# Kernel tuning notes

Measured on AMD Instinct MI355X. Metric: run time of the kernel, lower is better.

Reference implementation:

```python
import jax, jax.numpy as jnp
import numpy as np

RRELU_SLOPE = (1.0 / 8.0 + 1.0 / 3.0) / 2.0  # F.rrelu eval mode
N_ENT, N_REL2, H, E, B, T = 20000, 460, 128, 400000, 1024, 8


def _lin(x, W, b):
    return x @ W.T + b  # torch nn.Linear convention


def _gru_cell(x, h, w_ih, w_hh, b_ih, b_hh):
    gi = x @ w_ih.T + b_ih
    gh = h @ w_hh.T + b_hh
    i_r, i_z, i_n = jnp.split(gi, 3, axis=1)
    h_r, h_z, h_n = jnp.split(gh, 3, axis=1)
    r = jax.nn.sigmoid(i_r + h_r)
    z = jax.nn.sigmoid(i_z + h_z)
    n = jnp.tanh(i_n + r * h_n)
    return (1.0 - z) * n + z * h


def setup_inputs() -> dict:
    key = jax.random.key(0)
    ks = jax.random.split(key, 24)
    s = 0.02
    inp = {
        'ent_emb': jax.random.normal(ks[0], (N_ENT, H), jnp.float32),
        'rel_emb': jax.random.normal(ks[1], (N_REL2, H), jnp.float32),
        'weight_neighbor': jax.random.normal(ks[2], (H, H), jnp.float32) * s,
        'loop_weight': jax.random.normal(ks[3], (H, H), jnp.float32) * s,
        'evolve_loop_weight': jax.random.normal(ks[4], (H, H), jnp.float32) * s,
        'w_ih': jax.random.normal(ks[5], (3 * H, H), jnp.float32) * s,
        'w_hh': jax.random.normal(ks[6], (3 * H, H), jnp.float32) * s,
        'b_ih': jnp.zeros((3 * H,), jnp.float32),
        'b_hh': jnp.zeros((3 * H,), jnp.float32),
        'W_map1': jax.random.normal(ks[7], (2 * H, H), jnp.float32) * s,
        'b_map1': jnp.zeros((2 * H,), jnp.float32),
        'W_map2': jax.random.normal(ks[8], (H, 2 * H), jnp.float32) * s,
        'b_map2': jnp.zeros((H,), jnp.float32),
        'W_h1': jax.random.normal(ks[9], (H, H), jnp.float32) * s,
        'b_h1': jnp.zeros((H,), jnp.float32),
        'W_h2': jax.random.normal(ks[10], (H, H), jnp.float32) * s,
        'b_h2': jnp.zeros((H,), jnp.float32),
        'W_align': jax.random.normal(ks[11], (H, H), jnp.float32) * s,
        'b_align': jnp.zeros((H,), jnp.float32),
        'W_attn': jax.random.normal(ks[12], (H, H), jnp.float32) * s,
        'b_attn': jnp.zeros((H,), jnp.float32),
    }
    u = jax.random.uniform(ks[13], (B, T * N_REL2), jnp.float32)
    mask = jax.random.uniform(ks[14], (B, T * N_REL2)) > 0.7  # sparse history
    inp['partial_embeding'] = u * mask
    inp['edge_src'] = jax.random.randint(ks[15], (E,), 0, N_ENT, jnp.int32)
    inp['edge_dst'] = jax.random.randint(ks[16], (E,), 0, N_ENT, jnp.int32)
    inp['edge_type'] = jax.random.randint(ks[17], (E,), 0, N_REL2, jnp.int32)
    sub = jax.random.randint(ks[18], (B,), 0, N_ENT, jnp.int32)
    rel = jax.random.randint(ks[19], (B,), 0, N_REL2, jnp.int32)
    obj = jax.random.randint(ks[20], (B,), 0, N_ENT, jnp.int32)
    inp['triples'] = jnp.stack([sub, rel, obj], axis=1)
    return inp


def reference(ent_emb, rel_emb, weight_neighbor, loop_weight, evolve_loop_weight,
              w_ih, w_hh, b_ih, b_hh, W_map1, b_map1, W_map2, b_map2,
              W_h1, b_h1, W_h2, b_h2, W_align, b_align, W_attn, b_attn,
              partial_embeding, edge_src, edge_dst, edge_type, triples):
    # ---- UnionRGCNLayer: gather-transform-scatter ----
    h = ent_emb
    msg = (h[edge_src] + rel_emb[edge_type]) @ weight_neighbor          # [E, H]
    agg = jax.ops.segment_sum(msg, edge_dst, num_segments=N_ENT)        # [N, H]
    deg = jax.ops.segment_sum(jnp.ones((edge_dst.shape[0],), h.dtype), edge_dst,
                              num_segments=N_ENT)
    norm = jnp.where(deg > 0, 1.0 / jnp.where(deg > 0, deg, 1.0), 0.0)[:, None]
    loop = jnp.where((deg > 0)[:, None], h @ loop_weight, h @ evolve_loop_weight)
    x = agg * norm + loop
    pre_emb = jnp.where(x >= 0, x, x * RRELU_SLOPE)                     # rrelu (eval)

    # ---- PathPredictor.forward_back ----
    mapped_rel = _lin(_lin(rel_emb, W_map1, b_map1), W_map2, b_map2)    # [2R, H]
    q_rel = mapped_rel[triples[:, 1]]                                   # [B, H]
    A = _lin(q_rel, W_attn, b_attn) @ mapped_rel.T                      # [B, 2R]
    hist = partial_embeding.reshape(B, T, N_REL2).transpose(1, 0, 2)    # [T, B, 2R]

    def step(gh, cur):
        attn = cur * A
        attn = jax.nn.softmax(jnp.where(attn == 0, -1e9, attn), axis=1)
        rel_path = attn @ mapped_rel                                    # [B, H]
        return _gru_cell(rel_path, gh, w_ih, w_hh, b_ih, b_hh), None

    gru_hidden, _ = jax.lax.scan(step, jnp.zeros((B, H), pre_emb.dtype), hist)
    predicted_hist = 0.1 * _lin(_lin(q_rel, W_h1, b_h1), W_h2, b_h2) + q_rel
    match_loss = jnp.mean((predicted_hist - gru_hidden) ** 2)

    # ---- forward_forth, distmult scoring ----
    gh2 = _gru_cell(q_rel, predicted_hist, w_ih, w_hh, b_ih, b_hh)      # [B, H]
    sub_emb = pre_emb[triples[:, 0]]
    aligned_all = _lin(pre_emb, W_align, b_align)                       # [N, H]
    score_ = (_lin(sub_emb, W_align, b_align) * gh2) @ aligned_all.T    # [B, N]
    score = jax.nn.sigmoid(score_)
    # BCE(score, one_hot(obj)) without materializing labels:
    logp = jax.nn.log_sigmoid(score_)
    log1mp = jax.nn.log_sigmoid(-score_)
    total = -jnp.sum(log1mp)
    rows = jnp.arange(B)
    total = total + jnp.sum(log1mp[rows, triples[:, 2]] - logp[rows, triples[:, 2]])
    path_loss = total / (B * N_ENT)
    return score, match_loss, path_loss
```

## Files before the change

kernel.cpp:

```cpp
#include <hip/hip_runtime.h>

typedef unsigned short u16;
typedef unsigned int u32;
typedef __attribute__((ext_vector_type(8))) short bf8v;
typedef __attribute__((ext_vector_type(4))) float f4v;

#define RRELU_SLOPE 0.22916666667f

__device__ inline float bf2f(u16 u){ unsigned int i = ((unsigned int)u) << 16; float f; __builtin_memcpy(&f, &i, 4); return f; }
__device__ inline u16 f2bf(float f){ unsigned int i; __builtin_memcpy(&i, &f, 4); unsigned int r = (i + 0x7fffu + ((i >> 16) & 1u)) >> 16; return (u16)r; }
__device__ inline float frcp(float x){ return __builtin_amdgcn_rcpf(x); }
__device__ inline float fsigm(float x){ return frcp(1.f + __expf(-x)); }
__device__ inline float ftanh(float x){ return 2.f * frcp(1.f + __expf(-2.f * x)) - 1.f; }

__global__ __launch_bounds__(256) void prep_k(
    const float* __restrict__ Wn, const float* __restrict__ Wl, const float* __restrict__ We,
    const float* __restrict__ wih, const float* __restrict__ whh,
    const float* __restrict__ m1, const float* __restrict__ m2,
    const float* __restrict__ h1, const float* __restrict__ h2,
    const float* __restrict__ attn, const float* __restrict__ alg, const float* __restrict__ rel,
    const float* __restrict__ ent, const float* __restrict__ bat, const float* __restrict__ bh1,
    const int* __restrict__ edst, int E,
    u16* __restrict__ Bcat, u16* __restrict__ wihb, u16* __restrict__ whhb,
    u16* __restrict__ m1b, u16* __restrict__ m2b, u16* __restrict__ h1b, u16* __restrict__ h2b,
    u16* __restrict__ attnb, u16* __restrict__ algb, u16* __restrict__ relb,
    u16* __restrict__ entb, float* __restrict__ bias2, int* __restrict__ hist)
{
    int id = blockIdx.x * 256 + threadIdx.x;
    if (id < 49152) {
        int n = id / 384, k = id % 384;
        float v = (k < 128) ? Wn[k*128 + n] : (k < 256 ? Wl[(k-128)*128 + n] : We[(k-256)*128 + n]);
        Bcat[id] = f2bf(v); return;
    }
    id -= 49152;
    if (id < 49152) { wihb[id] = f2bf(wih[id]); return; } id -= 49152;
    if (id < 49152) { whhb[id] = f2bf(whh[id]); return; } id -= 49152;
    if (id < 32768) { m1b[id]  = f2bf(m1[id]);  return; } id -= 32768;
    if (id < 32768) { m2b[id]  = f2bf(m2[id]);  return; } id -= 32768;
    if (id < 16384) { h1b[id]  = f2bf(h1[id]);  return; } id -= 16384;
    if (id < 16384) { h2b[id]  = f2bf(h2[id]);  return; } id -= 16384;
    if (id < 16384) { attnb[id]= f2bf(attn[id]);return; } id -= 16384;
    if (id < 16384) { algb[id] = f2bf(alg[id]); return; } id -= 16384;
    if (id < 58880) { relb[id] = f2bf(rel[id]); return; } id -= 58880;
    if (id < 2560000) { entb[id] = f2bf(ent[id]); return; } id -= 2560000;
    if (id < 256) { bias2[id] = (id < 128) ? bat[id] : bh1[id - 128]; return; } id -= 256;
    if (id < E) atomicAdd(&hist[edst[id]], 1);
}

__global__ __launch_bounds__(1024) void scan_k(
    const int* __restrict__ hist, int* __restrict__ starts, int* __restrict__ cursor)
{
    __shared__ int part[1024];
    int t = threadIdx.x;
    int base = t * 20;
    int s = 0;
    for (int j = 0; j < 20; ++j) { int idx = base + j; if (idx < 20000) s += hist[idx]; }
    part[t] = s;
    __syncthreads();
    for (int off = 1; off < 1024; off <<= 1) {
        int v = (t >= off) ? part[t - off] : 0;
        __syncthreads();
        part[t] += v;
        __syncthreads();
    }
    int run = (t > 0) ? part[t - 1] : 0;
    for (int j = 0; j < 20; ++j) {
        int idx = base + j;
        if (idx < 20000) { starts[idx] = run; cursor[idx] = run; run += hist[idx]; }
    }
    if (t == 1023) starts[20000] = run;
}

__global__ __launch_bounds__(256) void scatter_k(
    const int* __restrict__ src, const int* __restrict__ dst, const int* __restrict__ typ,
    int* __restrict__ cursor, int2* __restrict__ spack, int E)
{
    int e = blockIdx.x * 256 + threadIdx.x;
    if (e >= E) return;
    int d = dst[e];
    int p = atomicAdd(&cursor[d], 1);
    spack[p] = make_int2(src[e], typ[e]);
}

__global__ __launch_bounds__(64) void agg_acat_k(
    const int2* __restrict__ spack, const int* __restrict__ starts,
    const u32* __restrict__ hb, const u32* __restrict__ rb, u32* __restrict__ Acat32)
{
    int i = blockIdx.x;
    int lane = threadIdx.x;
    int s0 = starts[i], s1 = starts[i + 1];
    float sx = 0.f, sy = 0.f;
    int e = s0;
    for (; e + 4 <= s1; e += 4) {
        int2 st0 = spack[e], st1 = spack[e+1], st2 = spack[e+2], st3 = spack[e+3];
        u32 a0 = hb[(long)st0.x * 64 + lane]; u32 r0 = rb[(long)st0.y * 64 + lane];
        u32 a1 = hb[(long)st1.x * 64 + lane]; u32 r1 = rb[(long)st1.y * 64 + lane];
        u32 a2 = hb[(long)st2.x * 64 + lane]; u32 r2 = rb[(long)st2.y * 64 + lane];
        u32 a3 = hb[(long)st3.x * 64 + lane]; u32 r3 = rb[(long)st3.y * 64 + lane];
        sx += bf2f((u16)(a0 & 0xffff)) + bf2f((u16)(r0 & 0xffff));
        sy += bf2f((u16)(a0 >> 16))    + bf2f((u16)(r0 >> 16));
        sx += bf2f((u16)(a1 & 0xffff)) + bf2f((u16)(r1 & 0xffff));
        sy += bf2f((u16)(a1 >> 16))    + bf2f((u16)(r1 >> 16));
        sx += bf2f((u16)(a2 & 0xffff)) + bf2f((u16)(r2 & 0xffff));
        sy += bf2f((u16)(a2 >> 16))    + bf2f((u16)(r2 >> 16));
        sx += bf2f((u16)(a3 & 0xffff)) + bf2f((u16)(r3 & 0xffff));
        sy += bf2f((u16)(a3 >> 16))    + bf2f((u16)(r3 >> 16));
    }
    for (; e < s1; ++e) {
        int2 st = spack[e];
        u32 a = hb[(long)st.x * 64 + lane];
        u32 r = rb[(long)st.y * 64 + lane];
        sx += bf2f((u16)(a & 0xffff)) + bf2f((u16)(r & 0xffff));
        sy += bf2f((u16)(a >> 16))    + bf2f((u16)(r >> 16));
    }
    bool has = s1 > s0;
    float nrm = has ? frcp((float)(s1 - s0)) : 0.f;
    u32 hv = hb[(long)i * 64 + lane];
    u32 agg = (u32)f2bf(sx * nrm) | ((u32)f2bf(sy * nrm) << 16);
    long o = (long)i * 192 + lane;
    Acat32[o]       = agg;
    Acat32[o + 64]  = has ? hv : 0u;
    Acat32[o + 128] = has ? 0u : hv;
}

__global__ __launch_bounds__(256) void gemm_nt(
    const u16* __restrict__ A, const u16* __restrict__ B, const float* __restrict__ bias,
    float* __restrict__ Cf, u16* __restrict__ Cbf, u16* __restrict__ CT,
    const u16* __restrict__ residb, const int* __restrict__ arows,
    int M, int N, int K, int lda, int ldb, int ldc, int ldct, int arow_stride,
    float rscale, int epi)
{
    int tid = threadIdx.x;
    int wave = tid >> 6, lane = tid & 63;
    int ln = lane & 15, q = lane >> 4;
    int bm = blockIdx.y * 64 + wave * 16;
    int bn = blockIdx.x * 64;
    int am = bm + ln; if (am >= M) am = M - 1;
    long ar = arows ? (long)arows[(long)am * arow_stride] : (long)am;
    const u16* Ap = A + ar * lda;
    int br[4];
#pragma unroll
    for (int nt = 0; nt < 4; ++nt) { int n = bn + nt*16 + ln; br[nt] = (n < N) ? n : (N - 1); }
    f4v acc[4] = {};
    for (int kc = 0; kc < K; kc += 32) {
        bf8v af = *(const bf8v*)(Ap + kc + q*8);
#pragma unroll
        for (int nt = 0; nt < 4; ++nt) {
            bf8v bv = *(const bf8v*)(B + (long)br[nt]*ldb + kc + q*8);
            acc[nt] = __builtin_amdgcn_mfma_f32_16x16x32_bf16(af, bv, acc[nt], 0, 0, 0);
        }
    }
#pragma unroll
    for (int nt = 0; nt < 4; ++nt) {
        int n = bn + nt*16 + ln;
        if (n >= N) continue;
        float bv = bias ? bias[n] : 0.f;
#pragma unroll
        for (int r = 0; r < 4; ++r) {
            int m = bm + q*4 + r;
            if (m >= M) continue;
            float v = acc[nt][r] + bv;
            if (epi == 1) v = (v >= 0.f) ? v : v * RRELU_SLOPE;
            if (residb)  v = rscale * v + bf2f(residb[(long)m*ldc + n]);
            long ci = (long)m*ldc + n;
            if (Cf)  Cf[ci]  = v;
            if (Cbf) Cbf[ci] = f2bf(v);
            if (CT)  CT[(long)n*ldct + m] = f2bf(v);
        }
    }
}

__global__ __launch_bounds__(256) void fuse_map_k(
    const u16* __restrict__ relb, const u16* __restrict__ m1b, const float* __restrict__ bm1,
    const u16* __restrict__ m2b, const float* __restrict__ bm2,
    u16* __restrict__ mapb, u16* __restrict__ mapT)
{
    __shared__ u16 t1l[4][16][264];
    int tid = threadIdx.x;
    int wave = tid >> 6, lane = tid & 63;
    int ln = lane & 15, q = lane >> 4;
    int base = blockIdx.x * 64 + wave * 16;
    int arow = base + ln; if (arow > 459) arow = 459;
    const u16* Ap = relb + arow * 128;
    f4v acc1[16] = {};
    for (int kc = 0; kc < 128; kc += 32) {
        bf8v af = *(const bf8v*)(Ap + kc + q*8);
#pragma unroll
        for (int nt = 0; nt < 16; ++nt) {
            bf8v bv = *(const bf8v*)(m1b + (nt*16 + ln)*128 + kc + q*8);
            acc1[nt] = __builtin_amdgcn_mfma_f32_16x16x32_bf16(af, bv, acc1[nt], 0, 0, 0);
        }
    }
#pragma unroll
    for (int nt = 0; nt < 16; ++nt) {
        int n = nt*16 + ln;
        float bv = bm1[n];
#pragma unroll
        for (int r = 0; r < 4; ++r)
            t1l[wave][q*4 + r][n] = f2bf(acc1[nt][r] + bv);
    }
    f4v acc2[8] = {};
    for (int kc = 0; kc < 256; kc += 32) {
        bf8v af = *(const bf8v*)&t1l[wave][ln][kc + q*8];
#pragma unroll
        for (int nt = 0; nt < 8; ++nt) {
            bf8v bv = *(const bf8v*)(m2b + (nt*16 + ln)*256 + kc + q*8);
            acc2[nt] = __builtin_amdgcn_mfma_f32_16x16x32_bf16(af, bv, acc2[nt], 0, 0, 0);
        }
    }
#pragma unroll
    for (int nt = 0; nt < 8; ++nt) {
        int n = nt*16 + ln;
        float bv = bm2[n];
#pragma unroll
        for (int r = 0; r < 4; ++r) {
            int m = base + q*4 + r;
            if (m < 460) {
                u16 hv = f2bf(acc2[nt][r] + bv);
                mapb[m*128 + n] = hv;
                mapT[n*480 + m] = hv;
            }
        }
    }
}

__global__ __launch_bounds__(256) void fuse_qt_k(
    const u16* __restrict__ mapb, const int* __restrict__ trip,
    const u16* __restrict__ atb, const float* __restrict__ bias2,
    const u16* __restrict__ h2b, const float* __restrict__ bh2,
    u16* __restrict__ atq, float* __restrict__ pred, u16* __restrict__ X)
{
    __shared__ u16 th1l[4][16][136];
    int tid = threadIdx.x;
    int wave = tid >> 6, lane = tid & 63;
    int ln = lane & 15, q = lane >> 4;
    int base = blockIdx.x * 64 + wave * 16;
    int ar = trip[(base + ln)*3 + 1];
    const u16* Ap = mapb + ar * 128;
    int rm_[4];
#pragma unroll
    for (int r = 0; r < 4; ++r) rm_[r] = trip[(base + q*4 + r)*3 + 1];
    f4v acc1[16] = {};
    for (int kc = 0; kc < 128; kc += 32) {
        bf8v af = *(const bf8v*)(Ap + kc + q*8);
#pragma unroll
        for (int nt = 0; nt < 16; ++nt) {
            bf8v bv = *(const bf8v*)(atb + (nt*16 + ln)*128 + kc + q*8);
            acc1[nt] = __builtin_amdgcn_mfma_f32_16x16x32_bf16(af, bv, acc1[nt], 0, 0, 0);
        }
    }
#pragma unroll
    for (int nt = 0; nt < 16; ++nt) {
        int n = nt*16 + ln;
        float bv = bias2[n];
#pragma unroll
        for (int r = 0; r < 4; ++r) {
            int m = base + q*4 + r;
            float x = acc1[nt][r] + bv;
            if (nt < 8) {
                atq[m*128 + n] = f2bf(x);
                X[(long)(8192 + m)*128 + n] = mapb[rm_[r]*128 + n];
            } else th1l[wave][q*4 + r][n - 128] = f2bf(x);
        }
    }
    f4v acc2[8] = {};
    for (int kc = 0; kc < 128; kc += 32) {
        bf8v af = *(const bf8v*)&th1l[wave][ln][kc + q*8];
#pragma unroll
        for (int nt = 0; nt < 8; ++nt) {
            bf8v bv = *(const bf8v*)(h2b + (nt*16 + ln)*128 + kc + q*8);
            acc2[nt] = __builtin_amdgcn_mfma_f32_16x16x32_bf16(af, bv, acc2[nt], 0, 0, 0);
        }
    }
#pragma unroll
    for (int nt = 0; nt < 8; ++nt) {
        int n = nt*16 + ln;
        float bv = bh2[n];
#pragma unroll
        for (int r = 0; r < 4; ++r) {
            int m = base + q*4 + r;
            pred[(long)m*128 + n] = 0.1f * (acc2[nt][r] + bv) + bf2f(mapb[rm_[r]*128 + n]);
        }
    }
}

__global__ __launch_bounds__(256) void smrp_k(
    const float* __restrict__ Amat, const float* __restrict__ part,
    const u16* __restrict__ mapT, u16* __restrict__ X)
{
    __shared__ u16 xls[32][488];
    __shared__ float asl[4][464];
    int tid = threadIdx.x;
    int wave = tid >> 6, lane = tid & 63;
    int b0 = blockIdx.x * 4;
    for (int i = tid; i < 4*460; i += 256)
        asl[i/460][i%460] = Amat[(long)(b0 + i/460)*460 + i%460];
    __syncthreads();
    for (int j = 0; j < 8; ++j) {
        int rl = wave*8 + j;
        int t = rl >> 2, db = rl & 3;
        const float* crow = part + (long)(b0 + db)*3680 + t*460;
        float v[8], e[8];
        float m = -1e30f;
#pragma unroll
        for (int i = 0; i < 8; ++i) {
            int r = i*64 + lane;
            if (r < 460) {
                float x = crow[r] * asl[db][r];
                x = (x == 0.f) ? -1e9f : x;
                v[i] = x; m = fmaxf(m, x);
            } else v[i] = -1e30f;
        }
#pragma unroll
        for (int off = 32; off; off >>= 1) m = fmaxf(m, __shfl_xor(m, off));
        float sum = 0.f;
#pragma unroll
        for (int i = 0; i < 8; ++i) {
            int r = i*64 + lane;
            e[i] = 0.f;
            if (r < 460) { e[i] = __expf(v[i] - m); sum += e[i]; }
        }
#pragma unroll
        for (int off = 32; off; off >>= 1) sum += __shfl_xor(sum, off);
        float inv = frcp(sum);
#pragma unroll
        for (int i = 0; i < 8; ++i) {
            int r = i*64 + lane;
            if (r < 460)      xls[rl][r] = f2bf(e[i] * inv);
            else if (r < 488) xls[rl][r] = 0;
        }
    }
    __syncthreads();
    int ln = lane & 15, q = lane >> 4;
    f4v acc[2][2] = {};
    for (int kc = 0; kc < 480; kc += 32) {
        bf8v a[2], bfr[2];
#pragma unroll
        for (int mt = 0; mt < 2; ++mt)
            a[mt] = *(const bf8v*)&xls[mt*16 + ln][kc + q*8];
#pragma unroll
        for (int nt = 0; nt < 2; ++nt)
            bfr[nt] = *(const bf8v*)(mapT + (wave*32 + nt*16 + ln)*480 + kc + q*8);
#pragma unroll
        for (int mt = 0; mt < 2; ++mt)
#pragma unroll
            for (int nt = 0; nt < 2; ++nt)
                acc[mt][nt] = __builtin_amdgcn_mfma_f32_16x16x32_bf16(a[mt], bfr[nt], acc[mt][nt], 0, 0, 0);
    }
#pragma unroll
    for (int mt = 0; mt < 2; ++mt)
#pragma unroll
    for (int nt = 0; nt < 2; ++nt) {
        int n = wave*32 + nt*16 + ln;
#pragma unroll
        for (int r = 0; r < 4; ++r) {
            int rl = mt*16 + q*4 + r;
            long m = (long)(rl >> 2)*1024 + b0 + (rl & 3);
            X[m*128 + n] = f2bf(acc[mt][nt][r]);
        }
    }
}

__global__ __launch_bounds__(256, 1) void gru_k(
    const u16* __restrict__ X, const u16* __restrict__ wihb, const float* __restrict__ bih,
    const u16* __restrict__ whhb, const float* __restrict__ bhh,
    const float* __restrict__ pred, const float* __restrict__ subl,
    const u16* __restrict__ AL, const int* __restrict__ trip,
    u16* __restrict__ V, float* __restrict__ accp)
{
    __shared__ u16  hbf[16][136];
    __shared__ float hf [4][128];
    __shared__ float ghl[4][388];
    __shared__ float gil[4][388];
    __shared__ float redm[4], redo[4];
    int tid = threadIdx.x;
    int wave = tid >> 6, lane = tid & 63;
    int ln = lane & 15, q = lane >> 4;
    int bb = blockIdx.x * 4;
    for (int i = tid; i < 16*136; i += 256) hbf[i/136][i%136] = 0;
    for (int i = tid; i < 4*128; i += 256) hf[i>>7][i&127] = 0.f;
    bf8v bfrag[6][4], wfrag[6][4];
#pragma unroll
    for (int nt = 0; nt < 6; ++nt)
#pragma unroll
        for (int kc = 0; kc < 4; ++kc) {
            bfrag[nt][kc] = *(const bf8v*)(whhb + (long)(wave*96 + nt*16 + ln)*128 + kc*32 + q*8);
            wfrag[nt][kc] = *(const bf8v*)(wihb + (long)(wave*96 + nt*16 + ln)*128 + kc*32 + q*8);
        }
    int k = tid & 127;
    float cr = bih[k] + bhh[k];
    float cz = bih[128 + k] + bhh[128 + k];
    float bin_ = bih[256 + k], bhn = bhh[256 + k];
    __syncthreads();
    float msum = 0.f, osum = 0.f;
    for (int t = 0; t <= 8; ++t) {
        float pv[2];
#pragma unroll
        for (int it = 0; it < 2; ++it) {
            int m = it*2 + (tid >> 7);
            pv[it] = (t >= 7) ? pred[(long)(bb + m)*128 + k] : 0.f;
        }
        if (t == 8) {
#pragma unroll
            for (int it = 0; it < 2; ++it) {
                int m = it*2 + (tid >> 7);
                hf[m][k] = pv[it]; hbf[m][k] = f2bf(pv[it]);
            }
            __syncthreads();
        }
        long xr0 = (t < 8) ? ((long)t*1024 + bb) : (long)(8192 + bb);
        const u16* Xp = X + (xr0 + (ln & 3))*128;
        f4v gacc[6] = {};
        f4v acc[6] = {};
#pragma unroll
        for (int kc = 0; kc < 4; ++kc) {
            bf8v xf = *(const bf8v*)(Xp + kc*32 + q*8);
            bf8v af = *(const bf8v*)&hbf[ln][kc*32 + q*8];
#pragma unroll
            for (int nt = 0; nt < 6; ++nt) {
                gacc[nt] = __builtin_amdgcn_mfma_f32_16x16x32_bf16(xf, wfrag[nt][kc], gacc[nt], 0, 0, 0);
                acc[nt]  = __builtin_amdgcn_mfma_f32_16x16x32_bf16(af, bfrag[nt][kc], acc[nt],  0, 0, 0);
            }
        }
        if (q == 0) {
#pragma unroll
            for (int nt = 0; nt < 6; ++nt)
#pragma unroll
                for (int r = 0; r < 4; ++r) {
                    ghl[r][wave*96 + nt*16 + ln] = acc[nt][r];
                    gil[r][wave*96 + nt*16 + ln] = gacc[nt][r];
                }
        }
        __syncthreads();
#pragma unroll
        for (int it = 0; it < 2; ++it) {
            int m = it*2 + (tid >> 7);
            float rr = fsigm(gil[m][k] + ghl[m][k] + cr);
            float zz = fsigm(gil[m][128 + k] + ghl[m][128 + k] + cz);
            float nn = ftanh(gil[m][256 + k] + bin_ + rr * (ghl[m][256 + k] + bhn));
            float hn = (1.f - zz) * nn + zz * hf[m][k];
            if (t == 7) { float d = pv[it] - hn; msum += d*d; }
            if (t == 8) {
                u16 vb = f2bf(subl[(long)(bb + m)*128 + k] * hn);
                V[(long)(bb + m)*128 + k] = vb;
                int obj = trip[(bb + m)*3 + 2];
                osum += bf2f(vb) * bf2f(AL[(long)obj*128 + k]);
            } else { hf[m][k] = hn; hbf[m][k] = f2bf(hn); }
        }
        __syncthreads();
    }
#pragma unroll
    for (int off = 32; off; off >>= 1) { msum += __shfl_down(msum, off); osum += __shfl_down(osum, off); }
    if (lane == 0) { redm[wave] = msum; redo[wave] = osum; }
    __syncthreads();
    if (tid == 0) {
        atomicAdd(accp + 0, redm[0] + redm[1] + redm[2] + redm[3]);
        atomicAdd(accp + 2, -(redo[0] + redo[1] + redo[2] + redo[3]));
    }
}

__global__ __launch_bounds__(512) void score_k(
    const u16* __restrict__ V, const u16* __restrict__ AL,
    float* __restrict__ out, float* __restrict__ sp_acc, int N)
{
    __shared__ float stage[8][2048];
    int tid = threadIdx.x;
    int wave = tid >> 6, lane = tid & 63;
    int ln = lane & 15, q = lane >> 4;
    int bm = blockIdx.y * 128 + (wave >> 2) * 64;
    int bn = blockIdx.x * 128 + (wave & 3) * 32;
    bool valid = bn < N;
    int br[2];
#pragma unroll
    for (int nt = 0; nt < 2; ++nt) { int n = bn + nt*16 + ln; br[nt] = (n < N) ? n : (N - 1); }
    f4v acc[4][2] = {};
    for (int kc = 0; kc < 128; kc += 32) {
        bf8v a[4], b[2];
#pragma unroll
        for (int mt = 0; mt < 4; ++mt)
            a[mt] = *(const bf8v*)(V + (long)(bm + mt*16 + ln)*128 + kc + q*8);
#pragma unroll
        for (int nt = 0; nt < 2; ++nt)
            b[nt] = *(const bf8v*)(AL + (long)br[nt]*128 + kc + q*8);
#pragma unroll
        for (int mt = 0; mt < 4; ++mt)
#pragma unroll
            for (int nt = 0; nt < 2; ++nt)
                acc[mt][nt] = __builtin_amdgcn_mfma_f32_16x16x32_bf16(a[mt], b[nt], acc[mt][nt], 0, 0, 0);
    }
    float lsum = 0.f;
    float* st = stage[wave];
#pragma unroll
    for (int mt = 0; mt < 4; ++mt)
#pragma unroll
    for (int nt = 0; nt < 2; ++nt)
#pragma unroll
    for (int r = 0; r < 4; ++r) {
        float s = acc[mt][nt][r];
        float e = __expf(-fabsf(s));
        float d = 1.f + e;
        float inv = frcp(d);
        st[(mt*16 + q*4 + r)*32 + nt*16 + ln] = (s >= 0.f) ? inv : e * inv;
        lsum += fmaxf(s, 0.f) + __logf(d);
    }
    if (!valid) lsum = 0.f;
    if (valid) {
        int row0 = lane >> 3, c4 = (lane & 7) << 2;
#pragma unroll
        for (int i = 0; i < 8; ++i) {
            int row = i*8 + row0;
            f4v vv = *(const f4v*)&st[row*32 + c4];
            __builtin_nontemporal_store(vv, (f4v*)&out[(long)(bm + row)*N + bn + c4]);
        }
    }
#pragma unroll
    for (int off = 32; off; off >>= 1) lsum += __shfl_xor(lsum, off);
    __shared__ float red[8];
    if (lane == 0) red[wave] = lsum;
    __syncthreads();
    if (tid == 0) {
        float tsum = 0.f;
#pragma unroll
        for (int w = 0; w < 8; ++w) tsum += red[w];
        atomicAdd(sp_acc, tsum);
    }
}

__global__ void final_k(const float* __restrict__ acc, float* __restrict__ out)
{
    out[20480000] = acc[0] / (1024.f * 128.f);
    out[20480001] = (acc[1] + acc[2]) / (1024.f * 20000.f);
}

extern "C" void kernel_launch(void* const* d_in, const int* in_sizes, int n_in,
                              void* d_out, int out_size, void* d_ws, size_t ws_size,
                              hipStream_t stream)
{
    const float* ent  = (const float*)d_in[0];
    const float* rel  = (const float*)d_in[1];
    const float* Wn   = (const float*)d_in[2];
    const float* Wl   = (const float*)d_in[3];
    const float* We   = (const float*)d_in[4];
    const float* wih  = (const float*)d_in[5];
    const float* whh  = (const float*)d_in[6];
    const float* b_ih = (const float*)d_in[7];
    const float* b_hh = (const float*)d_in[8];
    const float* Wm1  = (const float*)d_in[9];
    const float* bm1  = (const float*)d_in[10];
    const float* Wm2  = (const float*)d_in[11];
    const float* bm2  = (const float*)d_in[12];
    const float* Wh1  = (const float*)d_in[13];
    const float* bh1  = (const float*)d_in[14];
    const float* Wh2  = (const float*)d_in[15];
    const float* bh2  = (const float*)d_in[16];
    const float* Wal  = (const float*)d_in[17];
    const float* bal  = (const float*)d_in[18];
    const float* Wat  = (const float*)d_in[19];
    const float* bat  = (const float*)d_in[20];
    const float* part = (const float*)d_in[21];
    const int* esrc   = (const int*)d_in[22];
    const int* edst   = (const int*)d_in[23];
    const int* etyp   = (const int*)d_in[24];
    const int* trip   = (const int*)d_in[25];
    float* out = (float*)d_out;
    const int E = in_sizes[22];

    char* ws = (char*)d_ws;
    size_t off = 0;
    auto alloc = [&](size_t bytes) { size_t o = off; off = (off + bytes + 255) & ~(size_t)255; return o; };

    size_t o_acc   = alloc(256);
    size_t o_hist  = alloc(20000 * 4);
    size_t o_mapT  = alloc(128 * 480 * 2);
    size_t zend = off;
    size_t o_starts= alloc(20004 * 4);
    size_t o_cur   = alloc(20000 * 4);
    size_t o_spack = alloc((size_t)E * 8);
    size_t o_entb  = alloc((size_t)20000 * 128 * 2);
    size_t o_acat  = alloc((size_t)20000 * 384 * 2);
    size_t o_pre   = alloc((size_t)20000 * 128 * 2);
    size_t o_aln   = alloc((size_t)20000 * 128 * 2);
    size_t o_bcat  = alloc(128 * 384 * 2);
    size_t o_wih   = alloc(384 * 128 * 2);
    size_t o_whh   = alloc(384 * 128 * 2);
    size_t o_m1    = alloc(256 * 128 * 2);
    size_t o_m2    = alloc(128 * 256 * 2);
    size_t o_ath   = alloc(2 * 128 * 128 * 2);
    size_t o_h2    = alloc(128 * 128 * 2);
    size_t o_al    = alloc(128 * 128 * 2);
    size_t o_rel   = alloc(460 * 128 * 2);
    size_t o_map   = alloc(460 * 128 * 2);
    size_t o_atq   = alloc(1024 * 128 * 2);
    size_t o_b2    = alloc(256 * 4);
    size_t o_pred  = alloc(1024 * 128 * 4);
    size_t o_amat  = alloc((size_t)1024 * 460 * 4);
    size_t o_X     = alloc((size_t)9216 * 128 * 2);
    size_t o_subl  = alloc(1024 * 128 * 4);
    size_t o_V     = alloc(1024 * 128 * 2);

    float* accp  = (float*)(ws + o_acc);
    int* histp   = (int*)(ws + o_hist);
    u16* mapT    = (u16*)(ws + o_mapT);
    int* startsp = (int*)(ws + o_starts);
    int* curp    = (int*)(ws + o_cur);
    int2* spack  = (int2*)(ws + o_spack);
    u16* entb    = (u16*)(ws + o_entb);
    u16* acat    = (u16*)(ws + o_acat);
    u16* preb    = (u16*)(ws + o_pre);
    u16* alnb    = (u16*)(ws + o_aln);
    u16* bcat    = (u16*)(ws + o_bcat);
    u16* wihb    = (u16*)(ws + o_wih);
    u16* whhb    = (u16*)(ws + o_whh);
    u16* m1b     = (u16*)(ws + o_m1);
    u16* m2b     = (u16*)(ws + o_m2);
    u16* atb     = (u16*)(ws + o_ath);
    u16* h1b     = atb + 128 * 128;
    u16* h2b     = (u16*)(ws + o_h2);
    u16* alb     = (u16*)(ws + o_al);
    u16* relb    = (u16*)(ws + o_rel);
    u16* mapb    = (u16*)(ws + o_map);
    u16* atqb    = (u16*)(ws + o_atq);
    float* bias2 = (float*)(ws + o_b2);
    float* predf = (float*)(ws + o_pred);
    float* amat  = (float*)(ws + o_amat);
    u16* Xb      = (u16*)(ws + o_X);
    float* subl  = (float*)(ws + o_subl);
    u16* Vb      = (u16*)(ws + o_V);

    hipMemsetAsync(ws, 0, zend, stream);

    int ptot = 2897664 + E;
    prep_k<<<(ptot + 255) / 256, 256, 0, stream>>>(
        Wn, Wl, We, wih, whh, Wm1, Wm2, Wh1, Wh2, Wat, Wal, rel,
        ent, bat, bh1, edst, E,
        bcat, wihb, whhb, m1b, m2b, h1b, h2b, atb, alb, relb,
        entb, bias2, histp);

    scan_k<<<1, 1024, 0, stream>>>(histp, startsp, curp);
    int eb = (E + 255) / 256;
    scatter_k<<<eb, 256, 0, stream>>>(esrc, edst, etyp, curp, spack, E);
    agg_acat_k<<<20000, 64, 0, stream>>>(spack, startsp, (const u32*)entb, (const u32*)relb, (u32*)acat);

    gemm_nt<<<dim3(2, 313), 256, 0, stream>>>(acat, bcat, nullptr, nullptr, preb, nullptr, nullptr, nullptr,
                                              20000, 128, 384, 384, 384, 128, 0, 0, 0.f, 1);
    gemm_nt<<<dim3(2, 313), 256, 0, stream>>>(preb, alb, bal, nullptr, alnb, nullptr, nullptr, nullptr,
                                              20000, 128, 128, 128, 128, 128, 0, 0, 0.f, 0);

    fuse_map_k<<<8, 256, 0, stream>>>(relb, m1b, bm1, m2b, bm2, mapb, mapT);

    fuse_qt_k<<<16, 256, 0, stream>>>(mapb, trip, atb, bias2, h2b, bh2, atqb, predf, Xb);

    gemm_nt<<<dim3(8, 16), 256, 0, stream>>>(atqb, mapb, nullptr, amat, nullptr, nullptr, nullptr, nullptr,
                                             1024, 460, 128, 128, 128, 460, 0, 0, 0.f, 0);

    smrp_k<<<256, 256, 0, stream>>>(amat, part, mapT, Xb);

    gemm_nt<<<dim3(2, 16), 256, 0, stream>>>(preb, alb, bal, subl, nullptr, nullptr, nullptr, trip,
                                             1024, 128, 128, 128, 128, 128, 0, 3, 0.f, 0);

    gru_k<<<256, 256, 0, stream>>>(Xb, wihb, b_ih, whhb, b_hh, predf, subl, alnb, trip, Vb, accp);

    score_k<<<dim3(157, 8), 512, 0, stream>>>(Vb, alnb, out, accp + 1, 20000);

    final_k<<<1, 1, 0, stream>>>(accp, out);

    (void)in_sizes; (void)n_in; (void)out_size; (void)ws_size;
}
```

Baseline: 436.9 us.

## Fuse GEMMs into consumer kernels and drop generic gemm_nt launches

Fuses the two back-to-back 20000-row GEMMs (pre-embedding with RReLU, then the align projection) into one kernel that keeps the RReLU tile in shared memory for the second MFMA pass. Also computes the attention-query times mapped-relation GEMM inside smrp_k, and the subject-align linear inside gru_k, which removes the amat and subl intermediate buffers and three kernel launches. The aim is to cut launch overhead and global round-trips. In exchange some work is duplicated or done with lower MFMA utilisation: smrp_k uses only 4 of 16 MFMA rows, and each block reloads weight fragments.

```diff
diff --git a/kernel.cpp b/kernel.cpp
--- a/kernel.cpp
+++ b/kernel.cpp
@@ -123,49 +123,57 @@
     Acat32[o + 128] = has ? 0u : hv;
 }
 
-__global__ __launch_bounds__(256) void gemm_nt(
-    const u16* __restrict__ A, const u16* __restrict__ B, const float* __restrict__ bias,
-    float* __restrict__ Cf, u16* __restrict__ Cbf, u16* __restrict__ CT,
-    const u16* __restrict__ residb, const int* __restrict__ arows,
-    int M, int N, int K, int lda, int ldb, int ldc, int ldct, int arow_stride,
-    float rscale, int epi)
-{
+__global__ __launch_bounds__(256) void prealn_k(
+    const u16* __restrict__ acat, const u16* __restrict__ bcat,
+    const u16* __restrict__ alb, const float* __restrict__ bal,
+    u16* __restrict__ preb, u16* __restrict__ alnb)
+{
+    __shared__ u16 pl[4][16][136];
     int tid = threadIdx.x;
     int wave = tid >> 6, lane = tid & 63;
     int ln = lane & 15, q = lane >> 4;
-    int bm = blockIdx.y * 64 + wave * 16;
-    int bn = blockIdx.x * 64;
-    int am = bm + ln; if (am >= M) am = M - 1;
-    long ar = arows ? (long)arows[(long)am * arow_stride] : (long)am;
-    const u16* Ap = A + ar * lda;
-    int br[4];
-#pragma unroll
-    for (int nt = 0; nt < 4; ++nt) { int n = bn + nt*16 + ln; br[nt] = (n < N) ? n : (N - 1); }
-    f4v acc[4] = {};
-    for (int kc = 0; kc < K; kc += 32) {
+    int bm = blockIdx.x * 64 + wave * 16;
+    int am = bm + ln; if (am > 19999) am = 19999;
+    const u16* Ap = acat + (long)am * 384;
+    f4v acc[8] = {};
+    for (int kc = 0; kc < 384; kc += 32) {
         bf8v af = *(const bf8v*)(Ap + kc + q*8);
 #pragma unroll
-        for (int nt = 0; nt < 4; ++nt) {
-            bf8v bv = *(const bf8v*)(B + (long)br[nt]*ldb + kc + q*8);
+        for (int nt = 0; nt < 8; ++nt) {
+            bf8v bv = *(const bf8v*)(bcat + (nt*16 + ln)*384 + kc + q*8);
             acc[nt] = __builtin_amdgcn_mfma_f32_16x16x32_bf16(af, bv, acc[nt], 0, 0, 0);
         }
     }
 #pragma unroll
-    for (int nt = 0; nt < 4; ++nt) {
-        int n = bn + nt*16 + ln;
-        if (n >= N) continue;
-        float bv = bias ? bias[n] : 0.f;
+    for (int nt = 0; nt < 8; ++nt) {
+        int n = nt*16 + ln;
 #pragma unroll
         for (int r = 0; r < 4; ++r) {
             int m = bm + q*4 + r;
-            if (m >= M) continue;
-            float v = acc[nt][r] + bv;
-            if (epi == 1) v = (v >= 0.f) ? v : v * RRELU_SLOPE;
-            if (residb)  v = rscale * v + bf2f(residb[(long)m*ldc + n]);
-            long ci = (long)m*ldc + n;
-            if (Cf)  Cf[ci]  = v;
-            if (Cbf) Cbf[ci] = f2bf(v);
-            if (CT)  CT[(long)n*ldct + m] = f2bf(v);
+            float v = acc[nt][r];
+            v = (v >= 0.f) ? v : v * RRELU_SLOPE;
+            u16 hv = f2bf(v);
+            pl[wave][q*4 + r][n] = hv;
+            if (m < 20000) preb[(long)m*128 + n] = hv;
+        }
+    }
+    f4v acc2[8] = {};
+    for (int kc = 0; kc < 128; kc += 32) {
+        bf8v af = *(const bf8v*)&pl[wave][ln][kc + q*8];
+#pragma unroll
+        for (int nt = 0; nt < 8; ++nt) {
+            bf8v bv = *(const bf8v*)(alb + (nt*16 + ln)*128 + kc + q*8);
+            acc2[nt] = __builtin_amdgcn_mfma_f32_16x16x32_bf16(af, bv, acc2[nt], 0, 0, 0);
+        }
+    }
+#pragma unroll
+    for (int nt = 0; nt < 8; ++nt) {
+        int n = nt*16 + ln;
+        float bv = bal[n];
+#pragma unroll
+        for (int r = 0; r < 4; ++r) {
+            int m = bm + q*4 + r;
+            if (m < 20000) alnb[(long)m*128 + n] = f2bf(acc2[nt][r] + bv);
         }
     }
 }
@@ -285,16 +293,37 @@
 }
 
 __global__ __launch_bounds__(256) void smrp_k(
-    const float* __restrict__ Amat, const float* __restrict__ part,
-    const u16* __restrict__ mapT, u16* __restrict__ X)
+    const u16* __restrict__ atq, const u16* __restrict__ mapb,
+    const float* __restrict__ part, const u16* __restrict__ mapT, u16* __restrict__ X)
 {
     __shared__ u16 xls[32][488];
     __shared__ float asl[4][464];
     int tid = threadIdx.x;
     int wave = tid >> 6, lane = tid & 63;
+    int ln = lane & 15, q = lane >> 4;
     int b0 = blockIdx.x * 4;
-    for (int i = tid; i < 4*460; i += 256)
-        asl[i/460][i%460] = Amat[(long)(b0 + i/460)*460 + i%460];
+    {
+        const u16* Ap = atq + (long)(b0 + (ln & 3)) * 128;
+        bf8v af[4];
+#pragma unroll
+        for (int kc = 0; kc < 4; ++kc) af[kc] = *(const bf8v*)(Ap + kc*32 + q*8);
+        for (int nt = wave; nt < 29; nt += 4) {
+            int brow = nt*16 + ln; if (brow > 459) brow = 459;
+            f4v acc = {};
+#pragma unroll
+            for (int kc = 0; kc < 4; ++kc) {
+                bf8v bv = *(const bf8v*)(mapb + (long)brow*128 + kc*32 + q*8);
+                acc = __builtin_amdgcn_mfma_f32_16x16x32_bf16(af[kc], bv, acc, 0, 0, 0);
+            }
+            if (q == 0) {
+                int n = nt*16 + ln;
+                if (n < 460) {
+#pragma unroll
+                    for (int r = 0; r < 4; ++r) asl[r][n] = acc[r];
+                }
+            }
+        }
+    }
     __syncthreads();
     for (int j = 0; j < 8; ++j) {
         int rl = wave*8 + j;
@@ -331,7 +360,6 @@
         }
     }
     __syncthreads();
-    int ln = lane & 15, q = lane >> 4;
     f4v acc[2][2] = {};
     for (int kc = 0; kc < 480; kc += 32) {
         bf8v a[2], bfr[2];
@@ -364,7 +392,8 @@
 __global__ __launch_bounds__(256, 1) void gru_k(
     const u16* __restrict__ X, const u16* __restrict__ wihb, const float* __restrict__ bih,
     const u16* __restrict__ whhb, const float* __restrict__ bhh,
-    const float* __restrict__ pred, const float* __restrict__ subl,
+    const float* __restrict__ pred,
+    const u16* __restrict__ preb, const u16* __restrict__ alb, const float* __restrict__ bal,
     const u16* __restrict__ AL, const int* __restrict__ trip,
     u16* __restrict__ V, float* __restrict__ accp)
 {
@@ -372,6 +401,7 @@
     __shared__ float hf [4][128];
     __shared__ float ghl[4][388];
     __shared__ float gil[4][388];
+    __shared__ float sll[4][132];
     __shared__ float redm[4], redo[4];
     int tid = threadIdx.x;
     int wave = tid >> 6, lane = tid & 63;
@@ -387,6 +417,28 @@
             bfrag[nt][kc] = *(const bf8v*)(whhb + (long)(wave*96 + nt*16 + ln)*128 + kc*32 + q*8);
             wfrag[nt][kc] = *(const bf8v*)(wihb + (long)(wave*96 + nt*16 + ln)*128 + kc*32 + q*8);
         }
+    {
+        const u16* Pp = preb + (long)trip[(bb + (ln & 3))*3 + 0] * 128;
+        f4v sacc[2] = {};
+#pragma unroll
+        for (int kc = 0; kc < 4; ++kc) {
+            bf8v pf = *(const bf8v*)(Pp + kc*32 + q*8);
+#pragma unroll
+            for (int nt = 0; nt < 2; ++nt) {
+                bf8v bv = *(const bf8v*)(alb + (long)(wave*32 + nt*16 + ln)*128 + kc*32 + q*8);
+                sacc[nt] = __builtin_amdgcn_mfma_f32_16x16x32_bf16(pf, bv, sacc[nt], 0, 0, 0);
+            }
+        }
+        if (q == 0) {
+#pragma unroll
+            for (int nt = 0; nt < 2; ++nt) {
+                int n = wave*32 + nt*16 + ln;
+                float bv = bal[n];
+#pragma unroll
+                for (int r = 0; r < 4; ++r) sll[r][n] = sacc[nt][r] + bv;
+            }
+        }
+    }
     int k = tid & 127;
     float cr = bih[k] + bhh[k];
     float cz = bih[128 + k] + bhh[128 + k];
@@ -441,7 +493,7 @@
             float hn = (1.f - zz) * nn + zz * hf[m][k];
             if (t == 7) { float d = pv[it] - hn; msum += d*d; }
             if (t == 8) {
-                u16 vb = f2bf(subl[(long)(bb + m)*128 + k] * hn);
+                u16 vb = f2bf(sll[m][k] * hn);
                 V[(long)(bb + m)*128 + k] = vb;
                 int obj = trip[(bb + m)*3 + 2];
                 osum += bf2f(vb) * bf2f(AL[(long)obj*128 + k]);
@@ -593,9 +645,7 @@
     size_t o_atq   = alloc(1024 * 128 * 2);
     size_t o_b2    = alloc(256 * 4);
     size_t o_pred  = alloc(1024 * 128 * 4);
-    size_t o_amat  = alloc((size_t)1024 * 460 * 4);
     size_t o_X     = alloc((size_t)9216 * 128 * 2);
-    size_t o_subl  = alloc(1024 * 128 * 4);
     size_t o_V     = alloc(1024 * 128 * 2);
 
     float* accp  = (float*)(ws + o_acc);
@@ -622,9 +672,7 @@
     u16* atqb    = (u16*)(ws + o_atq);
     float* bias2 = (float*)(ws + o_b2);
     float* predf = (float*)(ws + o_pred);
-    float* amat  = (float*)(ws + o_amat);
     u16* Xb      = (u16*)(ws + o_X);
-    float* subl  = (float*)(ws + o_subl);
     u16* Vb      = (u16*)(ws + o_V);
 
     hipMemsetAsync(ws, 0, zend, stream);
@@ -641,24 +689,15 @@
     scatter_k<<<eb, 256, 0, stream>>>(esrc, edst, etyp, curp, spack, E);
     agg_acat_k<<<20000, 64, 0, stream>>>(spack, startsp, (const u32*)entb, (const u32*)relb, (u32*)acat);
 
-    gemm_nt<<<dim3(2, 313), 256, 0, stream>>>(acat, bcat, nullptr, nullptr, preb, nullptr, nullptr, nullptr,
-                                              20000, 128, 384, 384, 384, 128, 0, 0, 0.f, 1);
-    gemm_nt<<<dim3(2, 313), 256, 0, stream>>>(preb, alb, bal, nullptr, alnb, nullptr, nullptr, nullptr,
-                                              20000, 128, 128, 128, 128, 128, 0, 0, 0.f, 0);
+    prealn_k<<<313, 256, 0, stream>>>(acat, bcat, alb, bal, preb, alnb);
 
     fuse_map_k<<<8, 256, 0, stream>>>(relb, m1b, bm1, m2b, bm2, mapb, mapT);
 
     fuse_qt_k<<<16, 256, 0, stream>>>(mapb, trip, atb, bias2, h2b, bh2, atqb, predf, Xb);
 
-    gemm_nt<<<dim3(8, 16), 256, 0, stream>>>(atqb, mapb, nullptr, amat, nullptr, nullptr, nullptr, nullptr,
-                                             1024, 460, 128, 128, 128, 460, 0, 0, 0.f, 0);
-
-    smrp_k<<<256, 256, 0, stream>>>(amat, part, mapT, Xb);
-
-    gemm_nt<<<dim3(2, 16), 256, 0, stream>>>(preb, alb, bal, subl, nullptr, nullptr, nullptr, trip,
-                                             1024, 128, 128, 128, 128, 128, 0, 3, 0.f, 0);
-
-    gru_k<<<256, 256, 0, stream>>>(Xb, wihb, b_ih, whhb, b_hh, predf, subl, alnb, trip, Vb, accp);
+    smrp_k<<<256, 256, 0, stream>>>(atqb, mapb, part, mapT, Xb);
+
+    gru_k<<<256, 256, 0, stream>>>(Xb, wihb, b_ih, whhb, b_hh, predf, preb, alb, bal, alnb, trip, Vb, accp);
 
     score_k<<<dim3(157, 8), 512, 0, stream>>>(Vb, alnb, out, accp + 1, 20000);
 
```

Result: faster. 427.5 us (-2.1%).
